# Kernel optimization log

Hardware: AMD Instinct MI355X
Metric: run time of the kernel (lower is better)

## Reference

```python
import jax, jax.numpy as jnp
import numpy as np
from jax import lax

S, B, VIN, VOUT, U, E = 64, 256, 128, 128, 1024, 512
START_CODE = 0
T_DEC = 25  # MAX_DECODE_STEPS


def gru_step(x, h, Wih, Whh, bih, bhh):
    # PyTorch GRU cell, gate order r,z,n
    gi = x @ Wih.T + bih
    gh = h @ Whh.T + bhh
    ir, iz, inn = jnp.split(gi, 3, axis=-1)
    hr, hz, hn = jnp.split(gh, 3, axis=-1)
    r = jax.nn.sigmoid(ir + hr)
    z = jax.nn.sigmoid(iz + hz)
    n = jnp.tanh(inn + r * hn)
    return (1.0 - z) * n + z * h


def setup_inputs() -> dict:
    key = jax.random.key(0)
    ks = jax.random.split(key, 20)
    sc = 0.05
    inp = {
        'x': jax.random.normal(ks[0], (S, B, VIN), jnp.float32),
        'x_len': jnp.maximum(jnp.sort(jax.random.randint(ks[1], (B,), 0, S + 1)), 1),
        'enc_Wih': jax.random.normal(ks[2], (3 * U, VIN), jnp.float32) * sc,
        'enc_Whh': jax.random.normal(ks[3], (3 * U, U), jnp.float32) * sc,
        'enc_bih': jnp.zeros((3 * U,), jnp.float32),
        'enc_bhh': jnp.zeros((3 * U,), jnp.float32),
        'dec_Wih': jax.random.normal(ks[4], (3 * U, E + U), jnp.float32) * sc,
        'dec_Whh': jax.random.normal(ks[5], (3 * U, U), jnp.float32) * sc,
        'dec_bih': jnp.zeros((3 * U,), jnp.float32),
        'dec_bhh': jnp.zeros((3 * U,), jnp.float32),
        'o2h_W': jax.random.normal(ks[6], (E, VOUT), jnp.float32) * sc,
        'o2h_b': jnp.zeros((E,), jnp.float32),
        'fc_W': jax.random.normal(ks[7], (VOUT, U), jnp.float32) * sc,
        'fc_b': jnp.zeros((VOUT,), jnp.float32),
        'W1_W': jax.random.normal(ks[8], (U, U), jnp.float32) * sc,
        'W1_b': jnp.zeros((U,), jnp.float32),
        'W2_W': jax.random.normal(ks[9], (U, U), jnp.float32) * sc,
        'W2_b': jnp.zeros((U,), jnp.float32),
        'V_W': jax.random.normal(ks[10], (1, U), jnp.float32) * sc,
        'V_b': jnp.zeros((1,), jnp.float32),
    }
    return inp


def _forward(x, x_len, enc_Wih, enc_Whh, enc_bih, enc_bhh,
             dec_Wih, dec_Whh, dec_bih, dec_bhh,
             o2h_W, o2h_b, fc_W, fc_b, W1_W, W1_b, W2_W, W2_b, V_W, V_b):
    # ---- Encoder GRU with length masking (pack/pad semantics) ----
    h0 = jnp.zeros((B, U), jnp.float32)
    t_idx = jnp.arange(S)

    def enc_step(h, inp_t):
        xt, t = inp_t
        mask = (t < x_len)[:, None]  # [B,1]
        hn = gru_step(xt, h, enc_Wih, enc_Whh, enc_bih, enc_bhh)
        h = jnp.where(mask, hn, h)
        out = jnp.where(mask, hn, 0.0)
        return h, out

    enc_hidden, enc_out = lax.scan(enc_step, h0, (x, t_idx))  # enc_out [S,B,U]
    enc_out = jnp.transpose(enc_out, (1, 0, 2))  # [B,S,U]

    # ---- Greedy decode (teacher_force=False), 25 steps ----
    enc_proj = enc_out @ W1_W.T + W1_b  # precompute W1(enc_output), [B,S,U]
    start = jnp.zeros((B, VOUT), jnp.float32).at[:, START_CODE].set(1.0)

    def dec_step(carry, _):
        h, dec_in = carry
        score = jnp.tanh(enc_proj + (h @ W2_W.T + W2_b)[:, None, :])  # [B,S,U]
        logits = score @ V_W.T + V_b  # [B,S,1]
        attn = jax.nn.softmax(logits, axis=1)
        ctx = jnp.sum(attn * enc_out, axis=1)  # [B,U]
        emb = dec_in @ o2h_W.T + o2h_b  # [B,E]
        gx = jnp.concatenate([ctx, emb], axis=-1)
        hn = gru_step(gx, h, dec_Wih, dec_Whh, dec_bih, dec_bhh)
        pred = hn @ fc_W.T + fc_b  # [B,VOUT]
        onehot = jax.nn.one_hot(jnp.argmax(pred, axis=-1), VOUT, dtype=pred.dtype)
        return (hn, lax.stop_gradient(onehot)), pred

    _, preds = lax.scan(dec_step, (enc_hidden, start), None, length=T_DEC - 1)
    return jnp.concatenate([start[None], preds], axis=0)  # [25,B,VOUT]


def reference(x, x_len, enc_Wih, enc_Whh, enc_bih, enc_bhh,
              dec_Wih, dec_Whh, dec_bih, dec_bhh,
              o2h_W, o2h_b, fc_W, fc_b, W1_W, W1_b, W2_W, W2_b, V_W, V_b):
    return _forward(x, x_len, enc_Wih, enc_Whh, enc_bih, enc_bhh,
                    dec_Wih, dec_Whh, dec_bih, dec_bhh,
                    o2h_W, o2h_b, fc_W, fc_b, W1_W, W1_b, W2_W, W2_b, V_W, V_b)
```

## Files before the change

### kernel.cpp

```cpp
#include <hip/hip_runtime.h>
#include <math.h>

#define SLEN 64
#define BATCH 256
#define VIND 128
#define VOUTD 128
#define UDIM 1024
#define EDIM 512
#define TDEC 25
#define GXW 1536
#define U3 3072
#define NSEG 12

typedef __attribute__((ext_vector_type(8))) short short8;
typedef __attribute__((ext_vector_type(4))) float f32x4;

#define MFMA(acc, A, B) acc = __builtin_amdgcn_mfma_f32_16x16x32_bf16((A), (B), (acc), 0, 0, 0)

__device__ __forceinline__ float sigm(float x) { return 1.f / (1.f + expf(-x)); }

__device__ __forceinline__ float tanhf_fast(float x) {
    float ax = fabsf(x);
    float e = __expf(-2.f * ax);
    float t = (1.f - e) / (1.f + e);
    return copysignf(t, x);
}

__device__ __forceinline__ short f2bf(float f) {
    unsigned u = __float_as_uint(f);
    u += 0x7FFF + ((u >> 16) & 1);
    return (short)(u >> 16);
}
__device__ __forceinline__ float bf2f(short h) {
    return __uint_as_float(((unsigned)(unsigned short)h) << 16);
}

__device__ __forceinline__ size_t pkChunk(int r, int k, int K) {
    return ((size_t)(r >> 4) * (K >> 5) + (k >> 5)) * 64 + ((r & 15) + 16 * ((k >> 3) & 3));
}

union S8 { short s[8]; short8 v; };

__device__ __forceinline__ void writeSplit8(short* Hi, short* Lo, size_t chunk,
                                            const float* vals) {
    S8 h, l;
#pragma unroll
    for (int j = 0; j < 8; j++) {
        short hb = f2bf(vals[j]);
        h.s[j] = hb;
        l.s[j] = f2bf(vals[j] - bf2f(hb));
    }
    ((short8*)Hi)[chunk] = h.v;
    ((short8*)Lo)[chunk] = l.v;
}

__global__ void init_kernel(float* __restrict__ h0, short* __restrict__ hpHi,
                            short* __restrict__ hpLo, float* __restrict__ out0,
                            int* __restrict__ idx,
                            const float* __restrict__ o2h_W,
                            const float* __restrict__ o2h_b,
                            float* __restrict__ o2hT) {
    int i = blockIdx.x * 256 + threadIdx.x;
    if (i < BATCH * UDIM) { h0[i] = 0.f; hpHi[i] = 0; hpLo[i] = 0; }
    if (i < BATCH * VOUTD) out0[i] = ((i & (VOUTD - 1)) == 0) ? 1.f : 0.f;
    if (i < BATCH) idx[i] = 0;
    if (i < VOUTD * EDIM) {
        int v = i >> 9, e = i & (EDIM - 1);
        o2hT[i] = o2h_W[(size_t)e * VOUTD + v] + o2h_b[e];
    }
}

struct PackSeg {
    const float* sA; const float* sB;
    short* Hi; short* Lo;
    int KA, KB, offA, offB, chunkStart;
};
struct PackArgs { PackSeg s[NSEG]; };

__global__ void pack_all(PackArgs pa, int total) {
    int gid = blockIdx.x * 256 + threadIdx.x;
    if (gid >= total) return;
    int si = 0;
#pragma unroll
    for (int i = 1; i < NSEG; i++) si = (gid >= pa.s[i].chunkStart) ? i : si;
    PackSeg sg = pa.s[si];
    int local = gid - sg.chunkStart;
    int K = sg.KA + sg.KB;
    int cpr = K >> 3;
    int r = local / cpr, k0 = (local - r * cpr) * 8;
    const float* src = (k0 < sg.KA)
        ? sg.sA + (size_t)(sg.offA + r) * sg.KA + k0
        : sg.sB + (size_t)(sg.offB + r) * sg.KB + (k0 - sg.KA);
    float v[8];
#pragma unroll
    for (int j = 0; j < 8; j++) v[j] = src[j];
    writeSplit8(sg.Hi, sg.Lo, pkChunk(r, k0, K), v);
}

__global__ __launch_bounds__(256) void gemm_w(
    const short8* __restrict__ Ahi, const short8* __restrict__ Alo,
    const short8* __restrict__ Whi, const short8* __restrict__ Wlo,
    const float* __restrict__ bias, float* __restrict__ C,
    int KT, int N) {
    int tid = threadIdx.x, lane = tid & 63, wave = tid >> 6;
    int m16 = blockIdx.x * 4 + (wave & 1) * 2;
    int nb = blockIdx.y * 8 + (wave >> 1) * 4;
    const short8* a0h = Ahi + (size_t)m16 * KT * 64 + lane;
    const short8* a1h = a0h + (size_t)KT * 64;
    const short8* a0l = Alo + (size_t)m16 * KT * 64 + lane;
    const short8* a1l = a0l + (size_t)KT * 64;
    const short8* w0h = Whi + (size_t)(nb + 0) * KT * 64 + lane;
    const short8* w1h = Whi + (size_t)(nb + 1) * KT * 64 + lane;
    const short8* w2h = Whi + (size_t)(nb + 2) * KT * 64 + lane;
    const short8* w3h = Whi + (size_t)(nb + 3) * KT * 64 + lane;
    const short8* w0l = Wlo + (size_t)(nb + 0) * KT * 64 + lane;
    const short8* w1l = Wlo + (size_t)(nb + 1) * KT * 64 + lane;
    const short8* w2l = Wlo + (size_t)(nb + 2) * KT * 64 + lane;
    const short8* w3l = Wlo + (size_t)(nb + 3) * KT * 64 + lane;
    f32x4 acc0[4] = {}, acc1[4] = {};

    for (int kt = 0; kt < KT; kt++) {
        size_t o = (size_t)kt * 64;
        short8 A0H = a0h[o], A1H = a1h[o], A0L = a0l[o], A1L = a1l[o];
        short8 WH0 = w0h[o], WL0 = w0l[o];
        MFMA(acc0[0], A0H, WH0); MFMA(acc1[0], A1H, WH0);
        MFMA(acc0[0], A0H, WL0); MFMA(acc1[0], A1H, WL0);
        MFMA(acc0[0], A0L, WH0); MFMA(acc1[0], A1L, WH0);
        short8 WH1 = w1h[o], WL1 = w1l[o];
        MFMA(acc0[1], A0H, WH1); MFMA(acc1[1], A1H, WH1);
        MFMA(acc0[1], A0H, WL1); MFMA(acc1[1], A1H, WL1);
        MFMA(acc0[1], A0L, WH1); MFMA(acc1[1], A1L, WH1);
        short8 WH2 = w2h[o], WL2 = w2l[o];
        MFMA(acc0[2], A0H, WH2); MFMA(acc1[2], A1H, WH2);
        MFMA(acc0[2], A0H, WL2); MFMA(acc1[2], A1H, WL2);
        MFMA(acc0[2], A0L, WH2); MFMA(acc1[2], A1L, WH2);
        short8 WH3 = w3h[o], WL3 = w3l[o];
        MFMA(acc0[3], A0H, WH3); MFMA(acc1[3], A1H, WH3);
        MFMA(acc0[3], A0H, WL3); MFMA(acc1[3], A1H, WL3);
        MFMA(acc0[3], A0L, WH3); MFMA(acc1[3], A1L, WH3);
    }
    int rsub = (lane >> 4) * 4, cn = lane & 15;
    int row0 = (m16 + 0) * 16 + rsub;
    int row1 = (m16 + 1) * 16 + rsub;
#pragma unroll
    for (int j = 0; j < 4; j++) {
        int col = (nb + j) * 16 + cn;
        float bb = bias ? bias[col] : 0.f;
#pragma unroll
        for (int r = 0; r < 4; r++) {
            C[(size_t)(row0 + r) * N + col] = acc0[j][r] + bb;
            C[(size_t)(row1 + r) * N + col] = acc1[j][r] + bb;
        }
    }
}

__global__ __launch_bounds__(256) void gemm_bm32(
    const short8* __restrict__ Ahi, const short8* __restrict__ Alo,
    const short8* __restrict__ Whi, const short8* __restrict__ Wlo,
    const float* __restrict__ bias, float* __restrict__ C,
    int KT, int N) {
    int tid = threadIdx.x, lane = tid & 63, wave = tid >> 6;
    int m16 = blockIdx.x * 2 + (wave & 1);
    int n16 = blockIdx.y * 4 + (wave >> 1) * 2;
    const short8* ah = Ahi + (size_t)m16 * KT * 64 + lane;
    const short8* al = Alo + (size_t)m16 * KT * 64 + lane;
    const short8* w0h = Whi + (size_t)n16 * KT * 64 + lane;
    const short8* w1h = w0h + (size_t)KT * 64;
    const short8* w0l = Wlo + (size_t)n16 * KT * 64 + lane;
    const short8* w1l = w0l + (size_t)KT * 64;
    f32x4 a0 = {0,0,0,0}, a1 = {0,0,0,0};
    for (int kt = 0; kt < KT; kt++) {
        size_t o = (size_t)kt * 64;
        short8 AH = ah[o], AL = al[o];
        short8 W0H = w0h[o], W0L = w0l[o], W1H = w1h[o], W1L = w1l[o];
        MFMA(a0, AH, W0H); MFMA(a1, AH, W1H);
        MFMA(a0, AH, W0L); MFMA(a1, AH, W1L);
        MFMA(a0, AL, W0H); MFMA(a1, AL, W1H);
    }
    int rsub = (lane >> 4) * 4, cn = lane & 15;
    float b0 = bias ? bias[(n16 + 0) * 16 + cn] : 0.f;
    float b1 = bias ? bias[(n16 + 1) * 16 + cn] : 0.f;
#pragma unroll
    for (int r = 0; r < 4; r++) {
        int row = m16 * 16 + rsub + r;
        C[(size_t)row * N + (n16 + 0) * 16 + cn] = a0[r] + b0;
        C[(size_t)row * N + (n16 + 1) * 16 + cn] = a1[r] + b1;
    }
}

__global__ __launch_bounds__(384) void enc_gru3(
    const short8* __restrict__ hinH8, const short8* __restrict__ hinL8,
    const short8* __restrict__ WrH, const short8* __restrict__ WrL,
    const short8* __restrict__ WzH, const short8* __restrict__ WzL,
    const short8* __restrict__ WnH, const short8* __restrict__ WnL,
    const float* __restrict__ gi,
    const float* __restrict__ bih, const float* __restrict__ bhh,
    const float* __restrict__ hinF, float* __restrict__ houtF,
    short* __restrict__ hoH, short* __restrict__ hoL,
    short* __restrict__ eaHi, short* __restrict__ eaLo,
    const int* __restrict__ x_len, int t) {
    __shared__ float sC[6][16][16];
    __shared__ float sHo[16][16];
    __shared__ float sEo[16][16];
    int tid = threadIdx.x, lane = tid & 63, wave = tid >> 6;
    int g = blockIdx.x;
    int m16 = blockIdx.y;
    int gate = wave >> 1, half = wave & 1;
    const short8* ah = hinH8 + (size_t)m16 * 32 * 64 + (size_t)half * 16 * 64 + lane;
    const short8* al = hinL8 + (size_t)m16 * 32 * 64 + (size_t)half * 16 * 64 + lane;
    const short8* WH0 = (gate == 0) ? WrH : (gate == 1) ? WzH : WnH;
    const short8* WL0 = (gate == 0) ? WrL : (gate == 1) ? WzL : WnL;
    const short8* wh = WH0 + (size_t)g * 32 * 64 + (size_t)half * 16 * 64 + lane;
    const short8* wl = WL0 + (size_t)g * 32 * 64 + (size_t)half * 16 * 64 + lane;
    f32x4 acc = {0, 0, 0, 0};
    for (int kt = 0; kt < 16; kt++) {
        size_t o = (size_t)kt * 64;
        short8 AH = ah[o], AL = al[o];
        short8 WH = wh[o], WL = wl[o];
        MFMA(acc, AH, WH);
        MFMA(acc, AH, WL);
        MFMA(acc, AL, WH);
    }
    {
        int rsub = (lane >> 4) << 2, cn = lane & 15;
#pragma unroll
        for (int j = 0; j < 4; j++) sC[wave][rsub + j][cn] = acc[j];
    }
    __syncthreads();
    if (wave == 0) {
        int cu = g * 16 + (lane & 15);
        int rsub = (lane >> 4) << 2;
        float b_r = bih[cu] + bhh[cu];
        float b_z = bih[UDIM + cu] + bhh[UDIM + cu];
        float b_nh = bhh[2 * UDIM + cu];
        float b_ni = bih[2 * UDIM + cu];
        int growLocal = (t & 7) * 256;
#pragma unroll
        for (int j = 0; j < 4; j++) {
            int rr = rsub + j, cc = lane & 15;
            int b = m16 * 16 + rr;
            const float* gr = gi + (size_t)(growLocal + b) * U3;
            float rg = sigm(sC[0][rr][cc] + sC[1][rr][cc] + gr[cu] + b_r);
            float zg = sigm(sC[2][rr][cc] + sC[3][rr][cc] + gr[UDIM + cu] + b_z);
            float nn = tanhf(gr[2 * UDIM + cu] + b_ni +
                             rg * (sC[4][rr][cc] + sC[5][rr][cc] + b_nh));
            float hp = hinF[(size_t)b * UDIM + cu];
            float hv = (1.f - zg) * nn + zg * hp;
            bool msk = t < x_len[b];
            float ho = msk ? hv : hp;
            houtF[(size_t)b * UDIM + cu] = ho;
            sHo[rr][cc] = ho;
            sEo[rr][cc] = msk ? hv : 0.f;
        }
    }
    __syncthreads();
    if (wave == 1 && lane < 32) {
        int rr = lane >> 1, oct = lane & 1;
        int brow = m16 * 16 + rr;
        int u0 = g * 16 + oct * 8;
        float v[8];
#pragma unroll
        for (int j = 0; j < 8; j++) v[j] = sHo[rr][oct * 8 + j];
        writeSplit8(hoH, hoL, pkChunk(brow, u0, UDIM), v);
#pragma unroll
        for (int j = 0; j < 8; j++) v[j] = sEo[rr][oct * 8 + j];
        writeSplit8(eaHi, eaLo, pkChunk(brow * SLEN + t, u0, UDIM), v);
    }
}

__global__ __launch_bounds__(384) void dec_gru3(
    const short8* __restrict__ hinH8, const short8* __restrict__ hinL8,
    const short8* __restrict__ gxH8, const short8* __restrict__ gxL8,
    const short8* __restrict__ WrH, const short8* __restrict__ WrL,
    const short8* __restrict__ WzH, const short8* __restrict__ WzL,
    const short8* __restrict__ WnhH, const short8* __restrict__ WnhL,
    const short8* __restrict__ WniH, const short8* __restrict__ WniL,
    const float* __restrict__ bih, const float* __restrict__ bhh,
    const float* __restrict__ hinF, float* __restrict__ houtF,
    short* __restrict__ hoH, short* __restrict__ hoL) {
    __shared__ float sC[8][16][16];
    __shared__ float sHo[16][16];
    int tid = threadIdx.x, lane = tid & 63, wave = tid >> 6;
    int g = blockIdx.x;
    int m16 = blockIdx.y;
    int gate = wave >> 1, half = wave & 1;
    const short8* ah = hinH8 + (size_t)m16 * 32 * 64 + (size_t)half * 16 * 64 + lane;
    const short8* al = hinL8 + (size_t)m16 * 32 * 64 + (size_t)half * 16 * 64 + lane;
    const short8* gxh = gxH8 + (size_t)m16 * 48 * 64 + (size_t)half * 24 * 64 + lane;
    const short8* gxl = gxL8 + (size_t)m16 * 48 * 64 + (size_t)half * 24 * 64 + lane;
    const short8 *whA, *wlA, *whB, *wlB;
    if (gate == 0) {
        whA = WrH + (size_t)g * 80 * 64 + (size_t)half * 16 * 64 + lane;
        wlA = WrL + (size_t)g * 80 * 64 + (size_t)half * 16 * 64 + lane;
        whB = WrH + (size_t)g * 80 * 64 + (size_t)(32 + half * 24) * 64 + lane;
        wlB = WrL + (size_t)g * 80 * 64 + (size_t)(32 + half * 24) * 64 + lane;
    } else if (gate == 1) {
        whA = WzH + (size_t)g * 80 * 64 + (size_t)half * 16 * 64 + lane;
        wlA = WzL + (size_t)g * 80 * 64 + (size_t)half * 16 * 64 + lane;
        whB = WzH + (size_t)g * 80 * 64 + (size_t)(32 + half * 24) * 64 + lane;
        wlB = WzL + (size_t)g * 80 * 64 + (size_t)(32 + half * 24) * 64 + lane;
    } else {
        whA = WnhH + (size_t)g * 32 * 64 + (size_t)half * 16 * 64 + lane;
        wlA = WnhL + (size_t)g * 32 * 64 + (size_t)half * 16 * 64 + lane;
        whB = WniH + (size_t)g * 48 * 64 + (size_t)half * 24 * 64 + lane;
        wlB = WniL + (size_t)g * 48 * 64 + (size_t)half * 24 * 64 + lane;
    }
    f32x4 accA = {0,0,0,0}, accB = {0,0,0,0};
    for (int kt = 0; kt < 16; kt++) {
        size_t o = (size_t)kt * 64;
        short8 AH = ah[o], AL = al[o];
        short8 WH = whA[o], WL = wlA[o];
        MFMA(accA, AH, WH);
        MFMA(accA, AH, WL);
        MFMA(accA, AL, WH);
    }
    for (int kt = 0; kt < 24; kt++) {
        size_t o = (size_t)kt * 64;
        short8 AH = gxh[o], AL = gxl[o];
        short8 WH = whB[o], WL = wlB[o];
        MFMA(accB, AH, WH);
        MFMA(accB, AH, WL);
        MFMA(accB, AL, WH);
    }
    {
        int rsub = (lane >> 4) << 2, cn = lane & 15;
        if (wave < 4) {
#pragma unroll
            for (int j = 0; j < 4; j++) sC[wave][rsub + j][cn] = accA[j] + accB[j];
        } else {
#pragma unroll
            for (int j = 0; j < 4; j++) {
                sC[wave][rsub + j][cn] = accA[j];
                sC[wave + 2][rsub + j][cn] = accB[j];
            }
        }
    }
    __syncthreads();
    if (wave == 0) {
        int cu = g * 16 + (lane & 15);
        int rsub = (lane >> 4) << 2;
        float b_r = bih[cu] + bhh[cu];
        float b_z = bih[UDIM + cu] + bhh[UDIM + cu];
        float b_nh = bhh[2 * UDIM + cu];
        float b_ni = bih[2 * UDIM + cu];
#pragma unroll
        for (int j = 0; j < 4; j++) {
            int rr = rsub + j, cc = lane & 15;
            int b = m16 * 16 + rr;
            float rg = sigm(sC[0][rr][cc] + sC[1][rr][cc] + b_r);
            float zg = sigm(sC[2][rr][cc] + sC[3][rr][cc] + b_z);
            float nn = tanhf(sC[6][rr][cc] + sC[7][rr][cc] + b_ni +
                             rg * (sC[4][rr][cc] + sC[5][rr][cc] + b_nh));
            float hp = hinF[(size_t)b * UDIM + cu];
            float hv = (1.f - zg) * nn + zg * hp;
            houtF[(size_t)b * UDIM + cu] = hv;
            sHo[rr][cc] = hv;
        }
    }
    __syncthreads();
    if (wave == 1 && lane < 32) {
        int rr = lane >> 1, oct = lane & 1;
        int brow = m16 * 16 + rr;
        int u0 = g * 16 + oct * 8;
        float v[8];
#pragma unroll
        for (int j = 0; j < 8; j++) v[j] = sHo[rr][oct * 8 + j];
        writeSplit8(hoH, hoL, pkChunk(brow, u0, UDIM), v);
    }
}

__global__ __launch_bounds__(1024) void attn_ctx(
    const float* __restrict__ encProj,
    const short* __restrict__ eaHi, const short* __restrict__ eaLo,
    const float* __restrict__ tmp2, const float* __restrict__ V_W,
    const float* __restrict__ V_b,
    const float* __restrict__ o2hT,
    const int* __restrict__ idx, short* __restrict__ gxHi, short* __restrict__ gxLo) {
    int b = blockIdx.x;
    int tid = threadIdx.x, lane = tid & 63, wave = tid >> 6;
    __shared__ float s_t2[UDIM];
    __shared__ float s_v[UDIM];
    __shared__ float s_attn[SLEN];
    __shared__ float s_part[7][128][9];
    for (int u = tid; u < UDIM; u += 1024) {
        s_t2[u] = tmp2[(size_t)b * UDIM + u];
        s_v[u] = V_W[u];
    }
    __syncthreads();
    for (int s = wave; s < SLEN; s += 16) {
        const float4* ep4 = (const float4*)(encProj + ((size_t)b * SLEN + s) * UDIM);
        float p = 0.f;
        for (int u4 = lane; u4 < UDIM / 4; u4 += 64) {
            float4 e = ep4[u4];
            int u = 4 * u4;
            p += tanhf_fast(e.x + s_t2[u]) * s_v[u] +
                 tanhf_fast(e.y + s_t2[u + 1]) * s_v[u + 1] +
                 tanhf_fast(e.z + s_t2[u + 2]) * s_v[u + 2] +
                 tanhf_fast(e.w + s_t2[u + 3]) * s_v[u + 3];
        }
#pragma unroll
        for (int off = 32; off > 0; off >>= 1) p += __shfl_xor(p, off);
        if (lane == 0) s_attn[s] = p + V_b[0];
    }
    __syncthreads();
    if (tid < 64) {
        float v = s_attn[tid];
        float mx = v;
#pragma unroll
        for (int off = 32; off > 0; off >>= 1) mx = fmaxf(mx, __shfl_xor(mx, off));
        float e = expf(v - mx);
        float sum = e;
#pragma unroll
        for (int off = 32; off > 0; off >>= 1) sum += __shfl_xor(sum, off);
        s_attn[tid] = e / sum;
    }
    __syncthreads();
    {
        int grp = tid >> 7, tu = tid & 127;
        int u0 = tu * 8;
        float a[8] = {0, 0, 0, 0, 0, 0, 0, 0};
        const short8* hi8 = (const short8*)eaHi;
        const short8* lo8 = (const short8*)eaLo;
        int lanePart = 16 * ((u0 >> 3) & 3);
        int colPart = u0 >> 5;
        for (int s = grp * 8; s < grp * 8 + 8; s++) {
            int r = b * SLEN + s;
            size_t ch = ((size_t)(r >> 4) * (UDIM >> 5) + colPart) * 64 + (r & 15) + lanePart;
            S8 h, l;
            h.v = hi8[ch];
            l.v = lo8[ch];
            float w = s_attn[s];
#pragma unroll
            for (int j = 0; j < 8; j++) a[j] += w * (bf2f(h.s[j]) + bf2f(l.s[j]));
        }
        if (grp) {
#pragma unroll
            for (int j = 0; j < 8; j++) s_part[grp - 1][tu][j] = a[j];
        }
        __syncthreads();
        if (tid < 128) {
#pragma unroll
            for (int gg = 0; gg < 7; gg++)
#pragma unroll
                for (int j = 0; j < 8; j++) a[j] += s_part[gg][tu][j];
            writeSplit8(gxHi, gxLo, pkChunk(b, u0, GXW), a);
        } else if (tid < 192) {
            int e0 = (tid - 128) * 8;
            int ib = idx[b];
            const float* row = o2hT + (size_t)ib * EDIM + e0;
            float v[8];
#pragma unroll
            for (int j = 0; j < 8; j++) v[j] = row[j];
            writeSplit8(gxHi, gxLo, pkChunk(b, UDIM + e0, GXW), v);
        }
    }
}

__global__ __launch_bounds__(256) void fcw2(
    const short8* __restrict__ hHi, const short8* __restrict__ hLo,
    const short8* __restrict__ fcH, const short8* __restrict__ fcL,
    const float* __restrict__ fc_b, float* __restrict__ pred,
    int* __restrict__ idx,
    const short8* __restrict__ w2H, const short8* __restrict__ w2L,
    const float* __restrict__ W2_b, float* __restrict__ tmp2) {
    __shared__ float sP[16][129];
    int tid = threadIdx.x, lane = tid & 63, wave = tid >> 6;
    if (blockIdx.x < 16) {
        int fm = blockIdx.x;
        const short8* ah = hHi + (size_t)fm * 32 * 64 + lane;
        const short8* al = hLo + (size_t)fm * 32 * 64 + lane;
        int n0 = 2 * wave, n1 = 2 * wave + 1;
        const short8* w0h = fcH + (size_t)n0 * 32 * 64 + lane;
        const short8* w0l = fcL + (size_t)n0 * 32 * 64 + lane;
        const short8* w1h = fcH + (size_t)n1 * 32 * 64 + lane;
        const short8* w1l = fcL + (size_t)n1 * 32 * 64 + lane;
        f32x4 a0 = {0,0,0,0}, a1 = {0,0,0,0};
        for (int kt = 0; kt < 32; kt++) {
            size_t o = (size_t)kt * 64;
            short8 AH = ah[o], AL = al[o];
            short8 W0H = w0h[o], W0L = w0l[o], W1H = w1h[o], W1L = w1l[o];
            MFMA(a0, AH, W0H); MFMA(a1, AH, W1H);
            MFMA(a0, AH, W0L); MFMA(a1, AH, W1L);
            MFMA(a0, AL, W0H); MFMA(a1, AL, W1H);
        }
        int cn = lane & 15, rsub = (lane >> 4) << 2;
#pragma unroll
        for (int j = 0; j < 4; j++) {
            sP[rsub + j][n0 * 16 + cn] = a0[j] + fc_b[n0 * 16 + cn];
            sP[rsub + j][n1 * 16 + cn] = a1[j] + fc_b[n1 * 16 + cn];
        }
        __syncthreads();
        {
            int row = tid >> 4, c0 = (tid & 15) * 8;
            float* pr = pred + (size_t)(fm * 16 + row) * VOUTD;
#pragma unroll
            for (int j = 0; j < 8; j++) pr[c0 + j] = sP[row][c0 + j];
        }
        if (tid < 128) {
            int row = tid >> 3, seg = tid & 7;
            float v = -1e30f;
            int bi = 0;
            int c0 = seg * 16;
            for (int j = c0; j < c0 + 16; j++) {
                float w = sP[row][j];
                if (w > v) { v = w; bi = j; }
            }
#pragma unroll
            for (int off = 1; off < 8; off <<= 1) {
                float ov = __shfl_xor(v, off);
                int obi = __shfl_xor(bi, off);
                if (ov > v || (ov == v && obi < bi)) { v = ov; bi = obi; }
            }
            if (seg == 0) idx[fm * 16 + row] = bi;
        }
    } else {
        int lin = blockIdx.x - 16;
        int bx = lin & 7, by = lin >> 3;
        int m16 = bx * 2 + (wave & 1);
        int n16 = by * 4 + (wave >> 1) * 2;
        const short8* ah = hHi + (size_t)m16 * 32 * 64 + lane;
        const short8* al = hLo + (size_t)m16 * 32 * 64 + lane;
        const short8* w0h = w2H + (size_t)n16 * 32 * 64 + lane;
        const short8* w1h = w0h + (size_t)32 * 64;
        const short8* w0l = w2L + (size_t)n16 * 32 * 64 + lane;
        const short8* w1l = w0l + (size_t)32 * 64;
        f32x4 a0 = {0,0,0,0}, a1 = {0,0,0,0};
        for (int kt = 0; kt < 32; kt++) {
            size_t o = (size_t)kt * 64;
            short8 AH = ah[o], AL = al[o];
            short8 W0H = w0h[o], W0L = w0l[o], W1H = w1h[o], W1L = w1l[o];
            MFMA(a0, AH, W0H); MFMA(a1, AH, W1H);
            MFMA(a0, AH, W0L); MFMA(a1, AH, W1L);
            MFMA(a0, AL, W0H); MFMA(a1, AL, W1H);
        }
        int rsub = (lane >> 4) * 4, cn = lane & 15;
        float b0 = W2_b[(n16 + 0) * 16 + cn];
        float b1 = W2_b[(n16 + 1) * 16 + cn];
#pragma unroll
        for (int r = 0; r < 4; r++) {
            int row = m16 * 16 + rsub + r;
            tmp2[(size_t)row * UDIM + (n16 + 0) * 16 + cn] = a0[r] + b0;
            tmp2[(size_t)row * UDIM + (n16 + 1) * 16 + cn] = a1[r] + b1;
        }
    }
}

extern "C" void kernel_launch(void* const* d_in, const int* in_sizes, int n_in,
                              void* d_out, int out_size, void* d_ws, size_t ws_size,
                              hipStream_t stream) {
    const float* x       = (const float*)d_in[0];
    const int*   x_len   = (const int*)d_in[1];
    const float* enc_Wih = (const float*)d_in[2];
    const float* enc_Whh = (const float*)d_in[3];
    const float* enc_bih = (const float*)d_in[4];
    const float* enc_bhh = (const float*)d_in[5];
    const float* dec_Wih = (const float*)d_in[6];
    const float* dec_Whh = (const float*)d_in[7];
    const float* dec_bih = (const float*)d_in[8];
    const float* dec_bhh = (const float*)d_in[9];
    const float* o2h_W   = (const float*)d_in[10];
    const float* o2h_b   = (const float*)d_in[11];
    const float* fc_W    = (const float*)d_in[12];
    const float* fc_b    = (const float*)d_in[13];
    const float* W1_W    = (const float*)d_in[14];
    const float* W1_b    = (const float*)d_in[15];
    const float* W2_W    = (const float*)d_in[16];
    const float* W2_b    = (const float*)d_in[17];
    const float* V_W     = (const float*)d_in[18];
    const float* V_b     = (const float*)d_in[19];
    float* out = (float*)d_out;

    char* p = (char*)d_ws;
    auto alloc = [&](size_t bytes) -> char* {
        char* q = p;
        p += (bytes + 255) & ~(size_t)255;
        return q;
    };
    float* hAF  = (float*)alloc((size_t)BATCH * UDIM * 4);
    float* hBF  = (float*)alloc((size_t)BATCH * UDIM * 4);
    short* hAH  = (short*)alloc((size_t)BATCH * UDIM * 2);
    short* hAL  = (short*)alloc((size_t)BATCH * UDIM * 2);
    short* hBH  = (short*)alloc((size_t)BATCH * UDIM * 2);
    short* hBL  = (short*)alloc((size_t)BATCH * UDIM * 2);
    float* tmp2 = (float*)alloc((size_t)BATCH * UDIM * 4);
    short* gxHi = (short*)alloc((size_t)BATCH * GXW * 2);
    short* gxLo = (short*)alloc((size_t)BATCH * GXW * 2);
    short* encAHi = (short*)alloc((size_t)BATCH * SLEN * UDIM * 2);
    short* encALo = (short*)alloc((size_t)BATCH * SLEN * UDIM * 2);
    float* encProjF = (float*)alloc((size_t)BATCH * SLEN * UDIM * 4);
    float* gihBuf = (float*)alloc((size_t)8 * BATCH * U3 * 4);
    short* eWihH = (short*)alloc((size_t)U3 * VIND * 2);
    short* eWihL = (short*)alloc((size_t)U3 * VIND * 2);
    short* eWrH = (short*)alloc((size_t)UDIM * UDIM * 2);
    short* eWrL = (short*)alloc((size_t)UDIM * UDIM * 2);
    short* eWzH = (short*)alloc((size_t)UDIM * UDIM * 2);
    short* eWzL = (short*)alloc((size_t)UDIM * UDIM * 2);
    short* eWnH = (short*)alloc((size_t)UDIM * UDIM * 2);
    short* eWnL = (short*)alloc((size_t)UDIM * UDIM * 2);
    short* dWrH = (short*)alloc((size_t)UDIM * 2560 * 2);
    short* dWrL = (short*)alloc((size_t)UDIM * 2560 * 2);
    short* dWzH = (short*)alloc((size_t)UDIM * 2560 * 2);
    short* dWzL = (short*)alloc((size_t)UDIM * 2560 * 2);
    short* dWnhH = (short*)alloc((size_t)UDIM * UDIM * 2);
    short* dWnhL = (short*)alloc((size_t)UDIM * UDIM * 2);
    short* dWniH = (short*)alloc((size_t)UDIM * GXW * 2);
    short* dWniL = (short*)alloc((size_t)UDIM * GXW * 2);
    short* w1Hi = (short*)alloc((size_t)UDIM * UDIM * 2);
    short* w1Lo = (short*)alloc((size_t)UDIM * UDIM * 2);
    short* w2Hi = (short*)alloc((size_t)UDIM * UDIM * 2);
    short* w2Lo = (short*)alloc((size_t)UDIM * UDIM * 2);
    short* fcHi = (short*)alloc((size_t)VOUTD * UDIM * 2);
    short* fcLo = (short*)alloc((size_t)VOUTD * UDIM * 2);
    short* xHi  = (short*)alloc((size_t)SLEN * BATCH * VIND * 2);
    short* xLo  = (short*)alloc((size_t)SLEN * BATCH * VIND * 2);
    int*   idx  = (int*)alloc(BATCH * 4);
    float* o2hT = (float*)alloc((size_t)VOUTD * EDIM * 4);

    init_kernel<<<(BATCH * UDIM + 255) / 256, 256, 0, stream>>>(
        hAF, hAH, hAL, out, idx, o2h_W, o2h_b, o2hT);

    {
        PackArgs pa;
        int cs = 0, n = 0;
        auto seg = [&](const float* sA, int KA, int offA, const float* sB, int KB,
                       int offB, short* Hi, short* Lo, int R) {
            pa.s[n] = {sA, sB, Hi, Lo, KA, KB, offA, offB, cs};
            cs += R * (KA + KB) / 8;
            n++;
        };
        seg(enc_Wih, VIND, 0, nullptr, 0, 0, eWihH, eWihL, U3);
        seg(enc_Whh, UDIM, 0, nullptr, 0, 0, eWrH, eWrL, UDIM);
        seg(enc_Whh, UDIM, UDIM, nullptr, 0, 0, eWzH, eWzL, UDIM);
        seg(enc_Whh, UDIM, 2 * UDIM, nullptr, 0, 0, eWnH, eWnL, UDIM);
        seg(dec_Whh, UDIM, 0, dec_Wih, GXW, 0, dWrH, dWrL, UDIM);
        seg(dec_Whh, UDIM, UDIM, dec_Wih, GXW, UDIM, dWzH, dWzL, UDIM);
        seg(dec_Whh, UDIM, 2 * UDIM, nullptr, 0, 0, dWnhH, dWnhL, UDIM);
        seg(dec_Wih, GXW, 2 * UDIM, nullptr, 0, 0, dWniH, dWniL, UDIM);
        seg(W1_W, UDIM, 0, nullptr, 0, 0, w1Hi, w1Lo, UDIM);
        seg(W2_W, UDIM, 0, nullptr, 0, 0, w2Hi, w2Lo, UDIM);
        seg(fc_W, UDIM, 0, nullptr, 0, 0, fcHi, fcLo, VOUTD);
        seg(x, VIND, 0, nullptr, 0, 0, xHi, xLo, SLEN * BATCH);
        pack_all<<<(cs + 255) / 256, 256, 0, stream>>>(pa, cs);
    }

    float* hcF = hAF; float* hnF = hBF;
    short *hcH = hAH, *hcL = hAL, *hnH = hBH, *hnL = hBL;
    for (int c = 0; c < 8; c++) {
        gemm_w<<<dim3(32, 24), 256, 0, stream>>>(
            (const short8*)xHi + (size_t)c * 128 * 4 * 64,
            (const short8*)xLo + (size_t)c * 128 * 4 * 64,
            (const short8*)eWihH, (const short8*)eWihL,
            nullptr, gihBuf, VIND / 32, U3);
        for (int tt = 0; tt < 8; tt++) {
            int t = c * 8 + tt;
            enc_gru3<<<dim3(64, 16), 384, 0, stream>>>(
                (const short8*)hcH, (const short8*)hcL,
                (const short8*)eWrH, (const short8*)eWrL,
                (const short8*)eWzH, (const short8*)eWzL,
                (const short8*)eWnH, (const short8*)eWnL,
                gihBuf, enc_bih, enc_bhh, hcF, hnF, hnH, hnL,
                encAHi, encALo, x_len, t);
            { float* tf = hcF; hcF = hnF; hnF = tf; }
            { short* th = hcH; hcH = hnH; hnH = th; th = hcL; hcL = hnL; hnL = th; }
        }
    }

    gemm_w<<<dim3(SLEN * BATCH / 64, UDIM / 128), 256, 0, stream>>>(
        (const short8*)encAHi, (const short8*)encALo,
        (const short8*)w1Hi, (const short8*)w1Lo,
        W1_b, encProjF, UDIM / 32, UDIM);

    gemm_bm32<<<dim3(BATCH / 32, UDIM / 64), 256, 0, stream>>>(
        (const short8*)hcH, (const short8*)hcL,
        (const short8*)w2Hi, (const short8*)w2Lo,
        W2_b, tmp2, UDIM / 32, UDIM);

    for (int st = 0; st < TDEC - 1; st++) {
        attn_ctx<<<BATCH, 1024, 0, stream>>>(
            encProjF, encAHi, encALo, tmp2, V_W, V_b, o2hT, idx, gxHi, gxLo);
        dec_gru3<<<dim3(64, 16), 384, 0, stream>>>(
            (const short8*)hcH, (const short8*)hcL,
            (const short8*)gxHi, (const short8*)gxLo,
            (const short8*)dWrH, (const short8*)dWrL,
            (const short8*)dWzH, (const short8*)dWzL,
            (const short8*)dWnhH, (const short8*)dWnhL,
            (const short8*)dWniH, (const short8*)dWniL,
            dec_bih, dec_bhh, hcF, hnF, hnH, hnL);
        float* pred = out + (size_t)(1 + st) * BATCH * VOUTD;
        fcw2<<<144, 256, 0, stream>>>(
            (const short8*)hnH, (const short8*)hnL,
            (const short8*)fcHi, (const short8*)fcLo,
            fc_b, pred, idx,
            (const short8*)w2Hi, (const short8*)w2Lo, W2_b, tmp2);
        { float* tf = hcF; hcF = hnF; hnF = tf; }
        { short* th = hcH; hcH = hnH; hnH = th; th = hcL; hcL = hnL; hnL = th; }
    }
}
```

Before: 4.143 ms.

## Fuse decoder loop into one persistent cooperative kernel with grid syncs

Replaces the three per-step decoder launches (attention/context, GRU, fc+W2 projection) with a single cooperative persistent kernel of 256 blocks of 1024 threads. It loops over all 24 decode steps and uses grid.sync between phases instead of kernel boundaries. The GRU phase is remapped so each block does 4 m16 tiles with full-K waves instead of split-K halves. The aim is to remove launch overhead and inter-kernel gaps, at the cost of fewer active waves in the GRU and fc phases and the latency of grid-wide barriers.

```diff
diff --git a/kernel.cpp b/kernel.cpp
--- a/kernel.cpp
+++ b/kernel.cpp
@@ -1,5 +1,8 @@
 #include <hip/hip_runtime.h>
+#include <hip/hip_cooperative_groups.h>
 #include <math.h>
+
+namespace cg = cooperative_groups;
 
 #define SLEN 64
 #define BATCH 256
@@ -268,280 +271,280 @@
     }
 }
 
-__global__ __launch_bounds__(384) void dec_gru3(
-    const short8* __restrict__ hinH8, const short8* __restrict__ hinL8,
-    const short8* __restrict__ gxH8, const short8* __restrict__ gxL8,
-    const short8* __restrict__ WrH, const short8* __restrict__ WrL,
-    const short8* __restrict__ WzH, const short8* __restrict__ WzL,
-    const short8* __restrict__ WnhH, const short8* __restrict__ WnhL,
-    const short8* __restrict__ WniH, const short8* __restrict__ WniL,
-    const float* __restrict__ bih, const float* __restrict__ bhh,
-    const float* __restrict__ hinF, float* __restrict__ houtF,
-    short* __restrict__ hoH, short* __restrict__ hoL) {
-    __shared__ float sC[8][16][16];
-    __shared__ float sHo[16][16];
-    int tid = threadIdx.x, lane = tid & 63, wave = tid >> 6;
-    int g = blockIdx.x;
-    int m16 = blockIdx.y;
-    int gate = wave >> 1, half = wave & 1;
-    const short8* ah = hinH8 + (size_t)m16 * 32 * 64 + (size_t)half * 16 * 64 + lane;
-    const short8* al = hinL8 + (size_t)m16 * 32 * 64 + (size_t)half * 16 * 64 + lane;
-    const short8* gxh = gxH8 + (size_t)m16 * 48 * 64 + (size_t)half * 24 * 64 + lane;
-    const short8* gxl = gxL8 + (size_t)m16 * 48 * 64 + (size_t)half * 24 * 64 + lane;
-    const short8 *whA, *wlA, *whB, *wlB;
-    if (gate == 0) {
-        whA = WrH + (size_t)g * 80 * 64 + (size_t)half * 16 * 64 + lane;
-        wlA = WrL + (size_t)g * 80 * 64 + (size_t)half * 16 * 64 + lane;
-        whB = WrH + (size_t)g * 80 * 64 + (size_t)(32 + half * 24) * 64 + lane;
-        wlB = WrL + (size_t)g * 80 * 64 + (size_t)(32 + half * 24) * 64 + lane;
-    } else if (gate == 1) {
-        whA = WzH + (size_t)g * 80 * 64 + (size_t)half * 16 * 64 + lane;
-        wlA = WzL + (size_t)g * 80 * 64 + (size_t)half * 16 * 64 + lane;
-        whB = WzH + (size_t)g * 80 * 64 + (size_t)(32 + half * 24) * 64 + lane;
-        wlB = WzL + (size_t)g * 80 * 64 + (size_t)(32 + half * 24) * 64 + lane;
-    } else {
-        whA = WnhH + (size_t)g * 32 * 64 + (size_t)half * 16 * 64 + lane;
-        wlA = WnhL + (size_t)g * 32 * 64 + (size_t)half * 16 * 64 + lane;
-        whB = WniH + (size_t)g * 48 * 64 + (size_t)half * 24 * 64 + lane;
-        wlB = WniL + (size_t)g * 48 * 64 + (size_t)half * 24 * 64 + lane;
-    }
-    f32x4 accA = {0,0,0,0}, accB = {0,0,0,0};
-    for (int kt = 0; kt < 16; kt++) {
-        size_t o = (size_t)kt * 64;
-        short8 AH = ah[o], AL = al[o];
-        short8 WH = whA[o], WL = wlA[o];
-        MFMA(accA, AH, WH);
-        MFMA(accA, AH, WL);
-        MFMA(accA, AL, WH);
-    }
-    for (int kt = 0; kt < 24; kt++) {
-        size_t o = (size_t)kt * 64;
-        short8 AH = gxh[o], AL = gxl[o];
-        short8 WH = whB[o], WL = wlB[o];
-        MFMA(accB, AH, WH);
-        MFMA(accB, AH, WL);
-        MFMA(accB, AL, WH);
-    }
-    {
-        int rsub = (lane >> 4) << 2, cn = lane & 15;
-        if (wave < 4) {
-#pragma unroll
-            for (int j = 0; j < 4; j++) sC[wave][rsub + j][cn] = accA[j] + accB[j];
-        } else {
-#pragma unroll
-            for (int j = 0; j < 4; j++) {
-                sC[wave][rsub + j][cn] = accA[j];
-                sC[wave + 2][rsub + j][cn] = accB[j];
+struct DecArgs {
+    const float* encProj;
+    const short* eaHi; const short* eaLo;
+    float* tmp2;
+    const float* V_W; const float* V_b;
+    const float* o2hT;
+    int* idx;
+    short* gxHi; short* gxLo;
+    const short8 *dWrH, *dWrL, *dWzH, *dWzL, *dWnhH, *dWnhL, *dWniH, *dWniL;
+    const float *bih, *bhh;
+    float *hAF, *hBF;
+    short *hAH, *hAL, *hBH, *hBL;
+    const short8 *fcH, *fcL; const float* fc_b;
+    const short8 *w2H, *w2L; const float* W2_b;
+    float* out;
+};
+
+__global__ __launch_bounds__(1024, 4) void dec_persist(DecArgs A) {
+    cg::grid_group grid = cg::this_grid();
+    __shared__ union SMem {
+        struct { float t2[UDIM]; float v[UDIM]; float attn[SLEN]; float part[7][128][9]; } a;
+        struct { float sC[4][4][16][16]; float sHo[4][16][16]; } g;
+        struct { float sP[16][129]; } f;
+    } sm;
+    const int bid = blockIdx.x, tid = threadIdx.x, lane = tid & 63, w = tid >> 6;
+    const int gq = bid & 63, mq = bid >> 6;
+
+    for (int st = 0; st < TDEC - 1; st++) {
+        const float* hinF; float* houtF;
+        const short *hiH, *hiL; short *hoH, *hoL;
+        if (st & 1) { hinF = A.hBF; houtF = A.hAF; hiH = A.hBH; hiL = A.hBL; hoH = A.hAH; hoL = A.hAL; }
+        else        { hinF = A.hAF; houtF = A.hBF; hiH = A.hAH; hiL = A.hAL; hoH = A.hBH; hoL = A.hBL; }
+
+        {
+            const int b = bid;
+            for (int u = tid; u < UDIM; u += 1024) {
+                sm.a.t2[u] = A.tmp2[(size_t)b * UDIM + u];
+                sm.a.v[u] = A.V_W[u];
+            }
+            __syncthreads();
+            for (int s = w; s < SLEN; s += 16) {
+                const float4* ep4 = (const float4*)(A.encProj + ((size_t)b * SLEN + s) * UDIM);
+                float p = 0.f;
+                for (int u4 = lane; u4 < UDIM / 4; u4 += 64) {
+                    float4 e = ep4[u4];
+                    int u = 4 * u4;
+                    p += tanhf_fast(e.x + sm.a.t2[u]) * sm.a.v[u] +
+                         tanhf_fast(e.y + sm.a.t2[u + 1]) * sm.a.v[u + 1] +
+                         tanhf_fast(e.z + sm.a.t2[u + 2]) * sm.a.v[u + 2] +
+                         tanhf_fast(e.w + sm.a.t2[u + 3]) * sm.a.v[u + 3];
+                }
+#pragma unroll
+                for (int off = 32; off > 0; off >>= 1) p += __shfl_xor(p, off);
+                if (lane == 0) sm.a.attn[s] = p + A.V_b[0];
+            }
+            __syncthreads();
+            if (tid < 64) {
+                float v = sm.a.attn[tid];
+                float mx = v;
+#pragma unroll
+                for (int off = 32; off > 0; off >>= 1) mx = fmaxf(mx, __shfl_xor(mx, off));
+                float e = expf(v - mx);
+                float sum = e;
+#pragma unroll
+                for (int off = 32; off > 0; off >>= 1) sum += __shfl_xor(sum, off);
+                sm.a.attn[tid] = e / sum;
+            }
+            __syncthreads();
+            {
+                int grp = tid >> 7, tu = tid & 127;
+                int u0 = tu * 8;
+                float a[8] = {0, 0, 0, 0, 0, 0, 0, 0};
+                const short8* hi8 = (const short8*)A.eaHi;
+                const short8* lo8 = (const short8*)A.eaLo;
+                int lanePart = 16 * ((u0 >> 3) & 3);
+                int colPart = u0 >> 5;
+                for (int s = grp * 8; s < grp * 8 + 8; s++) {
+                    int r = b * SLEN + s;
+                    size_t ch = ((size_t)(r >> 4) * (UDIM >> 5) + colPart) * 64 + (r & 15) + lanePart;
+                    S8 h, l;
+                    h.v = hi8[ch];
+                    l.v = lo8[ch];
+                    float wt = sm.a.attn[s];
+#pragma unroll
+                    for (int j = 0; j < 8; j++) a[j] += wt * (bf2f(h.s[j]) + bf2f(l.s[j]));
+                }
+                if (grp) {
+#pragma unroll
+                    for (int j = 0; j < 8; j++) sm.a.part[grp - 1][tu][j] = a[j];
+                }
+                __syncthreads();
+                if (tid < 128) {
+#pragma unroll
+                    for (int gg = 0; gg < 7; gg++)
+#pragma unroll
+                        for (int j = 0; j < 8; j++) a[j] += sm.a.part[gg][tu][j];
+                    writeSplit8(A.gxHi, A.gxLo, pkChunk(b, u0, GXW), a);
+                } else if (tid < 192) {
+                    int e0 = (tid - 128) * 8;
+                    int ib = A.idx[b];
+                    const float* row = A.o2hT + (size_t)ib * EDIM + e0;
+                    float v[8];
+#pragma unroll
+                    for (int j = 0; j < 8; j++) v[j] = row[j];
+                    writeSplit8(A.gxHi, A.gxLo, pkChunk(b, UDIM + e0, GXW), v);
+                }
             }
         }
-    }
-    __syncthreads();
-    if (wave == 0) {
-        int cu = g * 16 + (lane & 15);
-        int rsub = (lane >> 4) << 2;
-        float b_r = bih[cu] + bhh[cu];
-        float b_z = bih[UDIM + cu] + bhh[UDIM + cu];
-        float b_nh = bhh[2 * UDIM + cu];
-        float b_ni = bih[2 * UDIM + cu];
-#pragma unroll
-        for (int j = 0; j < 4; j++) {
-            int rr = rsub + j, cc = lane & 15;
-            int b = m16 * 16 + rr;
-            float rg = sigm(sC[0][rr][cc] + sC[1][rr][cc] + b_r);
-            float zg = sigm(sC[2][rr][cc] + sC[3][rr][cc] + b_z);
-            float nn = tanhf(sC[6][rr][cc] + sC[7][rr][cc] + b_ni +
-                             rg * (sC[4][rr][cc] + sC[5][rr][cc] + b_nh));
-            float hp = hinF[(size_t)b * UDIM + cu];
-            float hv = (1.f - zg) * nn + zg * hp;
-            houtF[(size_t)b * UDIM + cu] = hv;
-            sHo[rr][cc] = hv;
+        __threadfence();
+        grid.sync();
+
+        {
+            if (w < 12) {
+                const int gate = w >> 2, mloc = w & 3, m16 = mq * 4 + mloc;
+                const short8* ah = (const short8*)hiH + (size_t)m16 * 32 * 64 + lane;
+                const short8* al = (const short8*)hiL + (size_t)m16 * 32 * 64 + lane;
+                const short8* gxh = (const short8*)A.gxHi + (size_t)m16 * 48 * 64 + lane;
+                const short8* gxl = (const short8*)A.gxLo + (size_t)m16 * 48 * 64 + lane;
+                const short8 *whA, *wlA, *whB, *wlB;
+                if (gate == 0) {
+                    whA = A.dWrH + (size_t)gq * 80 * 64 + lane; wlA = A.dWrL + (size_t)gq * 80 * 64 + lane;
+                    whB = whA + 32 * 64; wlB = wlA + 32 * 64;
+                } else if (gate == 1) {
+                    whA = A.dWzH + (size_t)gq * 80 * 64 + lane; wlA = A.dWzL + (size_t)gq * 80 * 64 + lane;
+                    whB = whA + 32 * 64; wlB = wlA + 32 * 64;
+                } else {
+                    whA = A.dWnhH + (size_t)gq * 32 * 64 + lane; wlA = A.dWnhL + (size_t)gq * 32 * 64 + lane;
+                    whB = A.dWniH + (size_t)gq * 48 * 64 + lane; wlB = A.dWniL + (size_t)gq * 48 * 64 + lane;
+                }
+                f32x4 accA = {0,0,0,0}, accB = {0,0,0,0};
+                for (int kt = 0; kt < 32; kt++) {
+                    size_t o = (size_t)kt * 64;
+                    short8 AH = ah[o], AL = al[o];
+                    short8 WH = whA[o], WL = wlA[o];
+                    MFMA(accA, AH, WH);
+                    MFMA(accA, AH, WL);
+                    MFMA(accA, AL, WH);
+                }
+                for (int kt = 0; kt < 48; kt++) {
+                    size_t o = (size_t)kt * 64;
+                    short8 AH = gxh[o], AL = gxl[o];
+                    short8 WH = whB[o], WL = wlB[o];
+                    MFMA(accB, AH, WH);
+                    MFMA(accB, AH, WL);
+                    MFMA(accB, AL, WH);
+                }
+                int rsub = (lane >> 4) << 2, cn = lane & 15;
+                if (gate < 2) {
+#pragma unroll
+                    for (int j = 0; j < 4; j++) sm.g.sC[mloc][gate][rsub + j][cn] = accA[j] + accB[j];
+                } else {
+#pragma unroll
+                    for (int j = 0; j < 4; j++) {
+                        sm.g.sC[mloc][2][rsub + j][cn] = accA[j];
+                        sm.g.sC[mloc][3][rsub + j][cn] = accB[j];
+                    }
+                }
+            }
+            __syncthreads();
+            if (w < 4) {
+                int m16 = mq * 4 + w;
+                int cu = gq * 16 + (lane & 15);
+                int rsub = (lane >> 4) << 2;
+                float b_r = A.bih[cu] + A.bhh[cu];
+                float b_z = A.bih[UDIM + cu] + A.bhh[UDIM + cu];
+                float b_nh = A.bhh[2 * UDIM + cu];
+                float b_ni = A.bih[2 * UDIM + cu];
+#pragma unroll
+                for (int j = 0; j < 4; j++) {
+                    int rr = rsub + j, cc = lane & 15;
+                    int b = m16 * 16 + rr;
+                    float rg = sigm(sm.g.sC[w][0][rr][cc] + b_r);
+                    float zg = sigm(sm.g.sC[w][1][rr][cc] + b_z);
+                    float nn = tanhf(sm.g.sC[w][3][rr][cc] + b_ni +
+                                     rg * (sm.g.sC[w][2][rr][cc] + b_nh));
+                    float hp = hinF[(size_t)b * UDIM + cu];
+                    float hv = (1.f - zg) * nn + zg * hp;
+                    houtF[(size_t)b * UDIM + cu] = hv;
+                    sm.g.sHo[w][rr][cc] = hv;
+                }
+            }
+            __syncthreads();
+            if (w >= 4 && w < 8 && lane < 32) {
+                int m16 = mq * 4 + (w - 4);
+                int rr = lane >> 1, oct = lane & 1;
+                int brow = m16 * 16 + rr;
+                int u0 = gq * 16 + oct * 8;
+                float v[8];
+#pragma unroll
+                for (int j = 0; j < 8; j++) v[j] = sm.g.sHo[w - 4][rr][oct * 8 + j];
+                writeSplit8(hoH, hoL, pkChunk(brow, u0, UDIM), v);
+            }
         }
-    }
-    __syncthreads();
-    if (wave == 1 && lane < 32) {
-        int rr = lane >> 1, oct = lane & 1;
-        int brow = m16 * 16 + rr;
-        int u0 = g * 16 + oct * 8;
-        float v[8];
-#pragma unroll
-        for (int j = 0; j < 8; j++) v[j] = sHo[rr][oct * 8 + j];
-        writeSplit8(hoH, hoL, pkChunk(brow, u0, UDIM), v);
-    }
-}
-
-__global__ __launch_bounds__(1024) void attn_ctx(
-    const float* __restrict__ encProj,
-    const short* __restrict__ eaHi, const short* __restrict__ eaLo,
-    const float* __restrict__ tmp2, const float* __restrict__ V_W,
-    const float* __restrict__ V_b,
-    const float* __restrict__ o2hT,
-    const int* __restrict__ idx, short* __restrict__ gxHi, short* __restrict__ gxLo) {
-    int b = blockIdx.x;
-    int tid = threadIdx.x, lane = tid & 63, wave = tid >> 6;
-    __shared__ float s_t2[UDIM];
-    __shared__ float s_v[UDIM];
-    __shared__ float s_attn[SLEN];
-    __shared__ float s_part[7][128][9];
-    for (int u = tid; u < UDIM; u += 1024) {
-        s_t2[u] = tmp2[(size_t)b * UDIM + u];
-        s_v[u] = V_W[u];
-    }
-    __syncthreads();
-    for (int s = wave; s < SLEN; s += 16) {
-        const float4* ep4 = (const float4*)(encProj + ((size_t)b * SLEN + s) * UDIM);
-        float p = 0.f;
-        for (int u4 = lane; u4 < UDIM / 4; u4 += 64) {
-            float4 e = ep4[u4];
-            int u = 4 * u4;
-            p += tanhf_fast(e.x + s_t2[u]) * s_v[u] +
-                 tanhf_fast(e.y + s_t2[u + 1]) * s_v[u + 1] +
-                 tanhf_fast(e.z + s_t2[u + 2]) * s_v[u + 2] +
-                 tanhf_fast(e.w + s_t2[u + 3]) * s_v[u + 3];
+        __threadfence();
+        grid.sync();
+
+        {
+            if (w < 4) {
+                int m16 = mq * 4 + w;
+                const short8* ah = (const short8*)hoH + (size_t)m16 * 32 * 64 + lane;
+                const short8* al = (const short8*)hoL + (size_t)m16 * 32 * 64 + lane;
+                const short8* wh = A.w2H + (size_t)gq * 32 * 64 + lane;
+                const short8* wl = A.w2L + (size_t)gq * 32 * 64 + lane;
+                f32x4 a0 = {0,0,0,0};
+                for (int kt = 0; kt < 32; kt++) {
+                    size_t o = (size_t)kt * 64;
+                    short8 AH = ah[o], AL = al[o];
+                    short8 WH = wh[o], WL = wl[o];
+                    MFMA(a0, AH, WH);
+                    MFMA(a0, AH, WL);
+                    MFMA(a0, AL, WH);
+                }
+                int rsub = (lane >> 4) << 2, cn = lane & 15;
+                float bb = A.W2_b[gq * 16 + cn];
+#pragma unroll
+                for (int r = 0; r < 4; r++) {
+                    int row = m16 * 16 + rsub + r;
+                    A.tmp2[(size_t)row * UDIM + gq * 16 + cn] = a0[r] + bb;
+                }
+            } else if (bid < 16 && w < 8) {
+                int wv = w - 4;
+                const short8* ah = (const short8*)hoH + (size_t)bid * 32 * 64 + lane;
+                const short8* al = (const short8*)hoL + (size_t)bid * 32 * 64 + lane;
+                int n0 = 2 * wv, n1 = 2 * wv + 1;
+                const short8* w0h = A.fcH + (size_t)n0 * 32 * 64 + lane;
+                const short8* w0l = A.fcL + (size_t)n0 * 32 * 64 + lane;
+                const short8* w1h = A.fcH + (size_t)n1 * 32 * 64 + lane;
+                const short8* w1l = A.fcL + (size_t)n1 * 32 * 64 + lane;
+                f32x4 a0 = {0,0,0,0}, a1 = {0,0,0,0};
+                for (int kt = 0; kt < 32; kt++) {
+                    size_t o = (size_t)kt * 64;
+                    short8 AH = ah[o], AL = al[o];
+                    short8 W0H = w0h[o], W0L = w0l[o], W1H = w1h[o], W1L = w1l[o];
+                    MFMA(a0, AH, W0H); MFMA(a1, AH, W1H);
+                    MFMA(a0, AH, W0L); MFMA(a1, AH, W1L);
+                    MFMA(a0, AL, W0H); MFMA(a1, AL, W1H);
+                }
+                int cn = lane & 15, rsub = (lane >> 4) << 2;
+#pragma unroll
+                for (int j = 0; j < 4; j++) {
+                    sm.f.sP[rsub + j][n0 * 16 + cn] = a0[j] + A.fc_b[n0 * 16 + cn];
+                    sm.f.sP[rsub + j][n1 * 16 + cn] = a1[j] + A.fc_b[n1 * 16 + cn];
+                }
+            }
+            __syncthreads();
+            if (bid < 16) {
+                if (tid < 256) {
+                    int row = tid >> 4, c0 = (tid & 15) * 8;
+                    float* pr = A.out + (size_t)(1 + st) * BATCH * VOUTD +
+                                (size_t)(bid * 16 + row) * VOUTD;
+#pragma unroll
+                    for (int j = 0; j < 8; j++) pr[c0 + j] = sm.f.sP[row][c0 + j];
+                }
+                if (tid < 128) {
+                    int row = tid >> 3, seg = tid & 7;
+                    float v = -1e30f;
+                    int bi = 0;
+                    int c0 = seg * 16;
+                    for (int j = c0; j < c0 + 16; j++) {
+                        float wv = sm.f.sP[row][j];
+                        if (wv > v) { v = wv; bi = j; }
+                    }
+#pragma unroll
+                    for (int off = 1; off < 8; off <<= 1) {
+                        float ov = __shfl_xor(v, off);
+                        int obi = __shfl_xor(bi, off);
+                        if (ov > v || (ov == v && obi < bi)) { v = ov; bi = obi; }
+                    }
+                    if (seg == 0) A.idx[bid * 16 + row] = bi;
+                }
+            }
         }
-#pragma unroll
-        for (int off = 32; off > 0; off >>= 1) p += __shfl_xor(p, off);
-        if (lane == 0) s_attn[s] = p + V_b[0];
-    }
-    __syncthreads();
-    if (tid < 64) {
-        float v = s_attn[tid];
-        float mx = v;
-#pragma unroll
-        for (int off = 32; off > 0; off >>= 1) mx = fmaxf(mx, __shfl_xor(mx, off));
-        float e = expf(v - mx);
-        float sum = e;
-#pragma unroll
-        for (int off = 32; off > 0; off >>= 1) sum += __shfl_xor(sum, off);
-        s_attn[tid] = e / sum;
-    }
-    __syncthreads();
-    {
-        int grp = tid >> 7, tu = tid & 127;
-        int u0 = tu * 8;
-        float a[8] = {0, 0, 0, 0, 0, 0, 0, 0};
-        const short8* hi8 = (const short8*)eaHi;
-        const short8* lo8 = (const short8*)eaLo;
-        int lanePart = 16 * ((u0 >> 3) & 3);
-        int colPart = u0 >> 5;
-        for (int s = grp * 8; s < grp * 8 + 8; s++) {
-            int r = b * SLEN + s;
-            size_t ch = ((size_t)(r >> 4) * (UDIM >> 5) + colPart) * 64 + (r & 15) + lanePart;
-            S8 h, l;
-            h.v = hi8[ch];
-            l.v = lo8[ch];
-            float w = s_attn[s];
-#pragma unroll
-            for (int j = 0; j < 8; j++) a[j] += w * (bf2f(h.s[j]) + bf2f(l.s[j]));
-        }
-        if (grp) {
-#pragma unroll
-            for (int j = 0; j < 8; j++) s_part[grp - 1][tu][j] = a[j];
-        }
-        __syncthreads();
-        if (tid < 128) {
-#pragma unroll
-            for (int gg = 0; gg < 7; gg++)
-#pragma unroll
-                for (int j = 0; j < 8; j++) a[j] += s_part[gg][tu][j];
-            writeSplit8(gxHi, gxLo, pkChunk(b, u0, GXW), a);
-        } else if (tid < 192) {
-            int e0 = (tid - 128) * 8;
-            int ib = idx[b];
-            const float* row = o2hT + (size_t)ib * EDIM + e0;
-            float v[8];
-#pragma unroll
-            for (int j = 0; j < 8; j++) v[j] = row[j];
-            writeSplit8(gxHi, gxLo, pkChunk(b, UDIM + e0, GXW), v);
-        }
-    }
-}
-
-__global__ __launch_bounds__(256) void fcw2(
-    const short8* __restrict__ hHi, const short8* __restrict__ hLo,
-    const short8* __restrict__ fcH, const short8* __restrict__ fcL,
-    const float* __restrict__ fc_b, float* __restrict__ pred,
-    int* __restrict__ idx,
-    const short8* __restrict__ w2H, const short8* __restrict__ w2L,
-    const float* __restrict__ W2_b, float* __restrict__ tmp2) {
-    __shared__ float sP[16][129];
-    int tid = threadIdx.x, lane = tid & 63, wave = tid >> 6;
-    if (blockIdx.x < 16) {
-        int fm = blockIdx.x;
-        const short8* ah = hHi + (size_t)fm * 32 * 64 + lane;
-        const short8* al = hLo + (size_t)fm * 32 * 64 + lane;
-        int n0 = 2 * wave, n1 = 2 * wave + 1;
-        const short8* w0h = fcH + (size_t)n0 * 32 * 64 + lane;
-        const short8* w0l = fcL + (size_t)n0 * 32 * 64 + lane;
-        const short8* w1h = fcH + (size_t)n1 * 32 * 64 + lane;
-        const short8* w1l = fcL + (size_t)n1 * 32 * 64 + lane;
-        f32x4 a0 = {0,0,0,0}, a1 = {0,0,0,0};
-        for (int kt = 0; kt < 32; kt++) {
-            size_t o = (size_t)kt * 64;
-            short8 AH = ah[o], AL = al[o];
-            short8 W0H = w0h[o], W0L = w0l[o], W1H = w1h[o], W1L = w1l[o];
-            MFMA(a0, AH, W0H); MFMA(a1, AH, W1H);
-            MFMA(a0, AH, W0L); MFMA(a1, AH, W1L);
-            MFMA(a0, AL, W0H); MFMA(a1, AL, W1H);
-        }
-        int cn = lane & 15, rsub = (lane >> 4) << 2;
-#pragma unroll
-        for (int j = 0; j < 4; j++) {
-            sP[rsub + j][n0 * 16 + cn] = a0[j] + fc_b[n0 * 16 + cn];
-            sP[rsub + j][n1 * 16 + cn] = a1[j] + fc_b[n1 * 16 + cn];
-        }
-        __syncthreads();
-        {
-            int row = tid >> 4, c0 = (tid & 15) * 8;
-            float* pr = pred + (size_t)(fm * 16 + row) * VOUTD;
-#pragma unroll
-            for (int j = 0; j < 8; j++) pr[c0 + j] = sP[row][c0 + j];
-        }
-        if (tid < 128) {
-            int row = tid >> 3, seg = tid & 7;
-            float v = -1e30f;
-            int bi = 0;
-            int c0 = seg * 16;
-            for (int j = c0; j < c0 + 16; j++) {
-                float w = sP[row][j];
-                if (w > v) { v = w; bi = j; }
-            }
-#pragma unroll
-            for (int off = 1; off < 8; off <<= 1) {
-                float ov = __shfl_xor(v, off);
-                int obi = __shfl_xor(bi, off);
-                if (ov > v || (ov == v && obi < bi)) { v = ov; bi = obi; }
-            }
-            if (seg == 0) idx[fm * 16 + row] = bi;
-        }
-    } else {
-        int lin = blockIdx.x - 16;
-        int bx = lin & 7, by = lin >> 3;
-        int m16 = bx * 2 + (wave & 1);
-        int n16 = by * 4 + (wave >> 1) * 2;
-        const short8* ah = hHi + (size_t)m16 * 32 * 64 + lane;
-        const short8* al = hLo + (size_t)m16 * 32 * 64 + lane;
-        const short8* w0h = w2H + (size_t)n16 * 32 * 64 + lane;
-        const short8* w1h = w0h + (size_t)32 * 64;
-        const short8* w0l = w2L + (size_t)n16 * 32 * 64 + lane;
-        const short8* w1l = w0l + (size_t)32 * 64;
-        f32x4 a0 = {0,0,0,0}, a1 = {0,0,0,0};
-        for (int kt = 0; kt < 32; kt++) {
-            size_t o = (size_t)kt * 64;
-            short8 AH = ah[o], AL = al[o];
-            short8 W0H = w0h[o], W0L = w0l[o], W1H = w1h[o], W1L = w1l[o];
-            MFMA(a0, AH, W0H); MFMA(a1, AH, W1H);
-            MFMA(a0, AH, W0L); MFMA(a1, AH, W1L);
-            MFMA(a0, AL, W0H); MFMA(a1, AL, W1H);
-        }
-        int rsub = (lane >> 4) * 4, cn = lane & 15;
-        float b0 = W2_b[(n16 + 0) * 16 + cn];
-        float b1 = W2_b[(n16 + 1) * 16 + cn];
-#pragma unroll
-        for (int r = 0; r < 4; r++) {
-            int row = m16 * 16 + rsub + r;
-            tmp2[(size_t)row * UDIM + (n16 + 0) * 16 + cn] = a0[r] + b0;
-            tmp2[(size_t)row * UDIM + (n16 + 1) * 16 + cn] = a1[r] + b1;
-        }
+        __threadfence();
+        grid.sync();
     }
 }
 
@@ -675,24 +678,29 @@
         (const short8*)w2Hi, (const short8*)w2Lo,
         W2_b, tmp2, UDIM / 32, UDIM);
 
-    for (int st = 0; st < TDEC - 1; st++) {
-        attn_ctx<<<BATCH, 1024, 0, stream>>>(
-            encProjF, encAHi, encALo, tmp2, V_W, V_b, o2hT, idx, gxHi, gxLo);
-        dec_gru3<<<dim3(64, 16), 384, 0, stream>>>(
-            (const short8*)hcH, (const short8*)hcL,
-            (const short8*)gxHi, (const short8*)gxLo,
-            (const short8*)dWrH, (const short8*)dWrL,
-            (const short8*)dWzH, (const short8*)dWzL,
-            (const short8*)dWnhH, (const short8*)dWnhL,
-            (const short8*)dWniH, (const short8*)dWniL,
-            dec_bih, dec_bhh, hcF, hnF, hnH, hnL);
-        float* pred = out + (size_t)(1 + st) * BATCH * VOUTD;
-        fcw2<<<144, 256, 0, stream>>>(
-            (const short8*)hnH, (const short8*)hnL,
-            (const short8*)fcHi, (const short8*)fcLo,
-            fc_b, pred, idx,
-            (const short8*)w2Hi, (const short8*)w2Lo, W2_b, tmp2);
-        { float* tf = hcF; hcF = hnF; hnF = tf; }
-        { short* th = hcH; hcH = hnH; hnH = th; th = hcL; hcL = hnL; hnL = th; }
-    }
-}
+    {
+        DecArgs da;
+        da.encProj = encProjF;
+        da.eaHi = encAHi; da.eaLo = encALo;
+        da.tmp2 = tmp2;
+        da.V_W = V_W; da.V_b = V_b;
+        da.o2hT = o2hT;
+        da.idx = idx;
+        da.gxHi = gxHi; da.gxLo = gxLo;
+        da.dWrH = (const short8*)dWrH; da.dWrL = (const short8*)dWrL;
+        da.dWzH = (const short8*)dWzH; da.dWzL = (const short8*)dWzL;
+        da.dWnhH = (const short8*)dWnhH; da.dWnhL = (const short8*)dWnhL;
+        da.dWniH = (const short8*)dWniH; da.dWniL = (const short8*)dWniL;
+        da.bih = dec_bih; da.bhh = dec_bhh;
+        da.hAF = hcF; da.hBF = hnF;
+        da.hAH = hcH; da.hAL = hcL; da.hBH = hnH; da.hBL = hnL;
+        da.fcH = (const short8*)fcHi; da.fcL = (const short8*)fcLo;
+        da.fc_b = fc_b;
+        da.w2H = (const short8*)w2Hi; da.w2L = (const short8*)w2Lo;
+        da.W2_b = W2_b;
+        da.out = out;
+        void* kparams[] = { (void*)&da };
+        hipLaunchCooperativeKernel(dec_persist, dim3(256), dim3(1024),
+                                   kparams, 0u, stream);
+    }
+}
```

After: 12.93 ms. 3.12x slower.
